# Kernel tuning notes

Hardware: AMD Instinct MI355X
Metric: run time of the kernel (lower is better)

The kernel has to match this reference:

```python
import jax, jax.numpy as jnp
import numpy as np

# Model dims (match init_kwargs / input_specs)
L = 2      # layer_dim
B = 64     # batch
T = 512    # max seq len
D = 256    # input_dim (== hidden_dim, required by stacked wiring)
H = 256    # hidden_dim
O = 2      # output_dim


def setup_inputs() -> dict:
    key = jax.random.key(0)
    ks = jax.random.split(key, 10)
    s = 1.0 / np.sqrt(H)
    f32 = jnp.float32
    return {
        "x_data": jax.random.normal(ks[0], (B, T, D), f32),
        "x_length": jax.random.randint(ks[1], (B,), 1, T + 1),
        "x_label": jax.random.uniform(ks[2], (B,), f32),
        # Per-layer GRU-cell weights, stacked over layers (bias=False).
        "Wz": (jax.random.normal(ks[3], (L, D, H), f32) * s),
        "Uz": (jax.random.normal(ks[4], (L, H, H), f32) * s),
        "Wr": (jax.random.normal(ks[5], (L, D, H), f32) * s),
        "Ur": (jax.random.normal(ks[6], (L, H, H), f32) * s),
        "Wh": (jax.random.normal(ks[7], (L, D, H), f32) * s),
        "Uh": (jax.random.normal(ks[8], (L, H, H), f32) * s),
        # Output projection of the last layer (only last layer's `out` is used).
        "Wo": (jax.random.normal(ks[9], (H, O), f32) * s),
    }


def reference(x_data, x_length, x_label, Wz, Uz, Wr, Ur, Wh, Uh, Wo):
    # Training-mode forward: sum over batch and valid timesteps of
    # (label - sigmoid(out[:, 1]))**2, with per-layer states S1, S2
    # carried across time. Vectorized over batch; lax.scan over time.
    Tn = x_data.shape[1]
    xs = jnp.swapaxes(x_data, 0, 1)  # [T, B, D]
    S1_0 = jnp.zeros((L, B, H), x_data.dtype)
    S2_0 = jnp.zeros((L, B, H), x_data.dtype)

    def step(carry, xt):
        S1, S2 = carry
        inp = xt  # [B, D]
        for l in range(L):  # small fixed layer loop
            z = jax.nn.sigmoid(inp @ Wz[l] + S1[l] @ Uz[l])
            r = jax.nn.sigmoid(inp @ Wr[l] + S1[l] @ Ur[l])
            h = jnp.tanh(inp @ Wh[l] + (r * S1[l]) @ Uh[l])
            hn = (1.0 - z) * S1[l] + z * h          # new hidden (S1)
            S2n = z * S2[l] + (1.0 - z) * h          # secondary memory (S2)
            S1 = S1.at[l].set(hn)
            S2 = S2.at[l].set(S2n)
            inp = hn
        score = jax.nn.sigmoid((inp @ Wo)[:, 1])     # out[:, 1] -> [B]
        return (S1, S2), score

    _, scores = jax.lax.scan(step, (S1_0, S2_0), xs)  # [T, B]
    mask = (jnp.arange(Tn)[:, None] < x_length[None, :]).astype(scores.dtype)
    loss = jnp.sum(mask * (x_label[None, :] - scores) ** 2)
    return loss
```

## Files before the change

kernel.cpp:

```cpp
#include <hip/hip_runtime.h>

#define LAY 2
#define BATCH 64
#define TMAX 512
#define DIM 256
#define AST 264
#define CHUNK 16

typedef float floatx4 __attribute__((ext_vector_type(4)));
typedef __bf16 bf16x8 __attribute__((ext_vector_type(8)));
#define MFMA_FP8  __builtin_amdgcn_mfma_f32_16x16x32_fp8_fp8
#define MFMA_BF16 __builtin_amdgcn_mfma_f32_16x16x32_bf16

#define BAR_LDS() asm volatile("s_waitcnt lgkmcnt(0)\n\ts_barrier" ::: "memory")

#define OFF_WPW 0x60000
#define OFF_FLG 0x150000
#define OFF_XP  0x200000
#define OFF_HP  0x1C00000
#define OFF_HN  0x3600000

__device__ __forceinline__ unsigned short f2bf(float f) {
    unsigned int u = __float_as_uint(f);
    unsigned int r = u + 0x7fffu + ((u >> 16) & 1u);
    return (unsigned short)(r >> 16);
}
__device__ __forceinline__ unsigned int pk2(float a, float b) {
    return (unsigned int)__builtin_amdgcn_cvt_pk_fp8_f32(a, b, 0, false);
}
__device__ __forceinline__ unsigned char f2q(float a) { return (unsigned char)(pk2(a, a) & 0xff); }
__device__ __forceinline__ void unp4(unsigned int u, float* f) {
    auto lo = __builtin_amdgcn_cvt_pk_f32_fp8((int)u, false);
    auto hi = __builtin_amdgcn_cvt_pk_f32_fp8((int)u, true);
    f[0] = lo[0]; f[1] = lo[1]; f[2] = hi[0]; f[3] = hi[1];
}
__device__ __forceinline__ float sigf(float x) {
    return __builtin_amdgcn_rcpf(1.f + __expf(-x));
}
__device__ __forceinline__ float tanhfast2y(float twoy) { return 2.f * sigf(twoy) - 1.f; }

__global__ void prep_weights(const float* __restrict__ Wz, const float* __restrict__ Wr,
                             const float* __restrict__ Wh, const float* __restrict__ Uz,
                             const float* __restrict__ Ur, const float* __restrict__ Uh,
                             unsigned char* __restrict__ ws, float* __restrict__ out) {
    int T = blockIdx.x * 256 + threadIdx.x;
    if (T == 0) out[0] = 0.f;
    if (T < 32) ((int*)(ws + OFF_FLG))[T] = 0;
    if (T < 196608) {
        int e = T & 3, half = (T >> 2) & 1, lane = (T >> 3) & 63;
        int kp = (T >> 9) & 3, nt = (T >> 11) & 15, mu = T >> 15;
        int g = mu % 3, l = mu / 3;
        const float* s = (g == 0 ? Uz : g == 1 ? Ur : Uh) + l * 65536;
        int n  = nt * 16 + (lane & 15);
        int k0 = (2 * kp + half) * 32 + (lane >> 4) * 8 + 2 * e;
        float w0 = s[(k0 << 8) + n] * 8.f;
        float w1 = s[((k0 + 1) << 8) + n] * 8.f;
        int addr = ((mu * 16 + nt) * 4 + kp) * 1024 + lane * 16 + half * 8 + 2 * e;
        *(unsigned short*)(ws + addr) = (unsigned short)(pk2(w0, w1) & 0xffff);
    } else {
        int T2 = T - 196608;
        int e = T2 & 3, lane = (T2 >> 2) & 63;
        int kf = (T2 >> 8) & 7, nt = (T2 >> 11) & 15, mw = T2 >> 15;
        int g = mw % 3, l = mw / 3;
        const float* s = (g == 0 ? Wz : g == 1 ? Wr : Wh) + l * 65536;
        int n  = nt * 16 + (lane & 15);
        int k0 = kf * 32 + (lane >> 4) * 8 + 2 * e;
        unsigned int v = (unsigned int)f2bf(s[(k0 << 8) + n]) |
                         ((unsigned int)f2bf(s[((k0 + 1) << 8) + n]) << 16);
        int addr = ((mw * 16 + nt) * 8 + kf) * 1024 + lane * 16 + 4 * e;
        *(unsigned int*)(ws + OFF_WPW + addr) = v;
    }
}

template <int F32SRC>
__global__ __launch_bounds__(1024) void proj_kernel(const void* __restrict__ src,
                                                    const unsigned char* __restrict__ wpW,
                                                    unsigned int* __restrict__ xpo, int matbase) {
    const int bgt = blockIdx.x;
    const int t = bgt & 511, bg = bgt >> 9;
    const int tid = threadIdx.x, wave = tid >> 6, lane = tid & 63;
    const int l15 = lane & 15, quad = lane >> 4;
    const size_t rowoff = ((size_t)(bg * 16 + l15) * 512 + t) * 256;

    bf16x8 af[8];
    if (F32SRC) {
        const float* s = (const float*)src + rowoff;
#pragma unroll
        for (int kf = 0; kf < 8; ++kf) {
            float4 a = *(const float4*)(s + kf * 32 + quad * 8);
            float4 b = *(const float4*)(s + kf * 32 + quad * 8 + 4);
            union { unsigned short u[8]; bf16x8 v; } cv;
            cv.u[0] = f2bf(a.x); cv.u[1] = f2bf(a.y); cv.u[2] = f2bf(a.z); cv.u[3] = f2bf(a.w);
            cv.u[4] = f2bf(b.x); cv.u[5] = f2bf(b.y); cv.u[6] = f2bf(b.z); cv.u[7] = f2bf(b.w);
            af[kf] = cv.v;
        }
    } else {
        const unsigned short* s = (const unsigned short*)src + rowoff;
#pragma unroll
        for (int kf = 0; kf < 8; ++kf) af[kf] = *(const bf16x8*)(s + kf * 32 + quad * 8);
    }

    floatx4 az = {0.f, 0.f, 0.f, 0.f}, ar = az, ah = az;
    const unsigned char* bz = wpW + (size_t)(((matbase + 0) * 16 + wave) * 8) * 1024 + lane * 16;
    const unsigned char* br = wpW + (size_t)(((matbase + 1) * 16 + wave) * 8) * 1024 + lane * 16;
    const unsigned char* bh = wpW + (size_t)(((matbase + 2) * 16 + wave) * 8) * 1024 + lane * 16;
#pragma unroll
    for (int kf = 0; kf < 8; ++kf) {
        az = MFMA_BF16(af[kf], *(const bf16x8*)(bz + kf * 1024), az, 0, 0, 0);
        ar = MFMA_BF16(af[kf], *(const bf16x8*)(br + kf * 1024), ar, 0, 0, 0);
        ah = MFMA_BF16(af[kf], *(const bf16x8*)(bh + kf * 1024), ah, 0, 0, 0);
    }
    const size_t ob = (size_t)bgt * 3072 + wave * 64 + lane;
    xpo[ob]        = pk2(16.f * az[0], 16.f * az[1]) | (pk2(16.f * az[2], 16.f * az[3]) << 16);
    xpo[ob + 1024] = pk2(16.f * ar[0], 16.f * ar[1]) | (pk2(16.f * ar[2], 16.f * ar[3]) << 16);
    xpo[ob + 2048] = pk2(16.f * ah[0], 16.f * ah[1]) | (pk2(16.f * ah[2], 16.f * ah[3]) << 16);
}

template <int SCORE, int WAIT, int POST>
__device__ __forceinline__ void scan_body(
    const unsigned int* __restrict__ xp, const unsigned char* __restrict__ wpU,
    int lbase, int bg, unsigned short* __restrict__ hnout,
    const int* __restrict__ xlen, const float* __restrict__ xlab,
    const float* __restrict__ Wo, float* __restrict__ out,
    int* wflags, int* pflag,
    unsigned char (*s1q)[AST], unsigned char (*rsq)[AST], float (*s1o)[264],
    float* wo1s, int* s_rdy, int tmax)
{
    const int tid = threadIdx.x, wave = tid >> 6, lane = tid & 63;
    const int l15 = lane & 15, quad = lane >> 4;
    const int b0 = bg * 16;

    for (int i = tid; i < 16 * AST; i += 1024) ((unsigned char*)s1q)[i] = 0;
    if (SCORE && tid < DIM) wo1s[tid] = Wo[2 * tid + 1];
    const int lenr = xlen[b0 + l15];
    const float labr = SCORE ? xlab[b0 + l15] : 0.f;
    (void)lenr; (void)labr;

    const int nt = wave;
    const int colA = nt * 16 + l15, rowb = quad * 4;

    long uz[8], ur[8], uh[8];
    {
        const unsigned char* pz = wpU + (size_t)(((lbase + 0) * 16 + nt) * 4) * 1024 + lane * 16;
        const unsigned char* pr = wpU + (size_t)(((lbase + 1) * 16 + nt) * 4) * 1024 + lane * 16;
        const unsigned char* ph = wpU + (size_t)(((lbase + 2) * 16 + nt) * 4) * 1024 + lane * 16;
#pragma unroll
        for (int kf = 0; kf < 8; ++kf) {
            int o = (kf >> 1) * 1024 + (kf & 1) * 8;
            uz[kf] = *(const long*)(pz + o);
            ur[kf] = *(const long*)(pr + o);
            uh[kf] = *(const long*)(ph + o);
        }
    }
    float s1r[4] = {};
    float accl = 0.f;
    int ready = 0;
    __syncthreads();

    for (int t = 0; t < tmax; ++t) {
        if (WAIT && t >= ready) {
            if (tid == 0) {
                int vv, g = 0;
                for (;;) {
                    int m0 = __hip_atomic_load(wflags + 0, __ATOMIC_RELAXED, __HIP_MEMORY_SCOPE_AGENT);
                    int m1 = __hip_atomic_load(wflags + 1, __ATOMIC_RELAXED, __HIP_MEMORY_SCOPE_AGENT);
                    int m2 = __hip_atomic_load(wflags + 2, __ATOMIC_RELAXED, __HIP_MEMORY_SCOPE_AGENT);
                    int m3 = __hip_atomic_load(wflags + 3, __ATOMIC_RELAXED, __HIP_MEMORY_SCOPE_AGENT);
                    int a = m0 < m1 ? m0 : m1, b = m2 < m3 ? m2 : m3;
                    vv = a < b ? a : b;
                    if (vv > t || ++g > (1 << 19)) break;
                    __builtin_amdgcn_s_sleep(2);
                }
                __threadfence();
                *s_rdy = vv > t ? vv : t + 1;
            }
            __syncthreads();
            ready = *s_rdy;
        }

        const unsigned int* xpt = xp + (size_t)(bg * 512 + t) * 3072 + lane;
        unsigned int xz = xpt[nt * 64];
        unsigned int xr = xpt[1024 + nt * 64];
        unsigned int xh = xpt[2048 + nt * 64];

        long sf[8];
#pragma unroll
        for (int kf = 0; kf < 8; ++kf) sf[kf] = *(const long*)&s1q[l15][kf * 32 + quad * 8];
        floatx4 za = {0.f, 0.f, 0.f, 0.f}, ra = za;
#pragma unroll
        for (int kf = 0; kf < 8; ++kf) {
            ra = MFMA_FP8(sf[kf], ur[kf], ra, 0, 0, 0);
            za = MFMA_FP8(sf[kf], uz[kf], za, 0, 0, 0);
        }
        float xrf[4];
        unp4(xr, xrf);
#pragma unroll
        for (int i = 0; i < 4; ++i) {
            float r = sigf(0.125f * ra[i] + 0.0625f * xrf[i]);
            rsq[rowb + i][colA] = f2q(r * s1r[i]);
        }
        BAR_LDS();

        long rf[8];
#pragma unroll
        for (int kf = 0; kf < 8; ++kf) rf[kf] = *(const long*)&rsq[l15][kf * 32 + quad * 8];
        floatx4 ha = {0.f, 0.f, 0.f, 0.f};
#pragma unroll
        for (int kf = 0; kf < 8; ++kf) ha = MFMA_FP8(rf[kf], uh[kf], ha, 0, 0, 0);
        float xzf[4], xhf[4];
        unp4(xz, xzf); unp4(xh, xhf);
#pragma unroll
        for (int i = 0; i < 4; ++i) {
            float z = sigf(0.125f * za[i] + 0.0625f * xzf[i]);
            float h = tanhfast2y(0.25f * ha[i] + 0.125f * xhf[i]);
            float hn = (1.f - z) * s1r[i] + z * h;
            s1r[i] = hn;
            s1q[rowb + i][colA] = f2q(hn);
            s1o[rowb + i][colA] = hn;
        }
        BAR_LDS();

        if (!SCORE) {
            const int r = tid >> 6, c = (tid & 63) * 4;
            float4 f0 = *(const float4*)&s1o[r][c];
            uint2 o2;
            o2.x = f2bf(f0.x) | ((unsigned)f2bf(f0.y) << 16);
            o2.y = f2bf(f0.z) | ((unsigned)f2bf(f0.w) << 16);
            *(uint2*)(hnout + ((size_t)(b0 + r) * 512 + t) * 256 + c) = o2;
        } else if (wave == 0) {
            const int row = l15, c0 = quad * 64;
            float p = 0.f;
#pragma unroll
            for (int u = 0; u < 64; u += 4) {
                float4 sv = *(const float4*)&s1o[row][c0 + u];
                float4 wv = *(const float4*)&wo1s[c0 + u];
                p = fmaf(sv.x, wv.x, p); p = fmaf(sv.y, wv.y, p);
                p = fmaf(sv.z, wv.z, p); p = fmaf(sv.w, wv.w, p);
            }
            p += __shfl_xor(p, 16);
            p += __shfl_xor(p, 32);
            if (lane < 16 && t < lenr) {
                float sc = sigf(p);
                float d = labr - sc;
                accl = fmaf(d, d, accl);
            }
        }

        if (POST && (((t & (CHUNK - 1)) == (CHUNK - 1)) || t == tmax - 1)) {
            __syncthreads();
            if (tid == 0) {
                __threadfence();
                __hip_atomic_store(pflag, t + 1, __ATOMIC_RELEASE, __HIP_MEMORY_SCOPE_AGENT);
            }
        }
    }

    if (SCORE && wave == 0) {
        accl += __shfl_xor(accl, 1);
        accl += __shfl_xor(accl, 2);
        accl += __shfl_xor(accl, 4);
        accl += __shfl_xor(accl, 8);
        if (lane == 0) atomicAdd(out, accl);
    }
}

__global__ __launch_bounds__(1024, 4) void fused_pipeline(
    const unsigned int* __restrict__ XP, unsigned int* __restrict__ HP,
    const unsigned char* __restrict__ wpU, const unsigned char* __restrict__ wpW,
    unsigned short* __restrict__ HN,
    const int* __restrict__ xlen, const float* __restrict__ xlab,
    const float* __restrict__ Wo, float* __restrict__ out, int* flags)
{
    __shared__ __align__(16) unsigned char s1q[16][AST];
    __shared__ __align__(16) unsigned char rsq[16][AST];
    __shared__ __align__(16) float s1o[16][264];
    __shared__ float wo1s[DIM];
    __shared__ int s_rdy;

    const int bid = blockIdx.x;
    int role, bg, p = 0;
    if (bid < 4)       { role = 0; bg = bid; }
    else if (bid < 20) { role = 1; bg = (bid - 4) >> 2; p = (bid - 4) & 3; }
    else               { role = 2; bg = bid - 20; }

    const int tid = threadIdx.x, wave = tid >> 6, lane = tid & 63;
    const int l15 = lane & 15, quad = lane >> 4;
    const int b0 = bg * 16;

    int v = xlen[b0 + l15];
#pragma unroll
    for (int o = 1; o < 16; o <<= 1) v = max(v, __shfl_xor(v, o));
    const int tmax = __builtin_amdgcn_readfirstlane(v);

    if (role == 0) {
        scan_body<0, 0, 1>(XP, wpU, 0, bg, HN, xlen, xlab, Wo, out,
                           nullptr, flags + bg, s1q, rsq, s1o, wo1s, &s_rdy, tmax);
    } else if (role == 2) {
        scan_body<1, 1, 0>(HP, wpU, 3, bg, nullptr, xlen, xlab, Wo, out,
                           flags + 4 + bg * 4, nullptr, s1q, rsq, s1o, wo1s, &s_rdy, tmax);
    } else {
        int* wf = flags + bg;
        int* pf = flags + 4 + bg * 4 + p;
        const unsigned char* bz = wpW + (size_t)(((3 + 0) * 16 + wave) * 8) * 1024 + lane * 16;
        const unsigned char* br = wpW + (size_t)(((3 + 1) * 16 + wave) * 8) * 1024 + lane * 16;
        const unsigned char* bh = wpW + (size_t)(((3 + 2) * 16 + wave) * 8) * 1024 + lane * 16;
        for (int base = 0; base < tmax; base += CHUNK) {
            const int target = (base + CHUNK < tmax) ? base + CHUNK : tmax;
            if (tid == 0) {
                int vv, g = 0;
                for (;;) {
                    vv = __hip_atomic_load(wf, __ATOMIC_RELAXED, __HIP_MEMORY_SCOPE_AGENT);
                    if (vv >= target || ++g > (1 << 19)) break;
                    __builtin_amdgcn_s_sleep(2);
                }
                __threadfence();
            }
            __syncthreads();

            const int t0 = base + p * 4;
            const int t1 = (t0 + 4 < tmax) ? t0 + 4 : tmax;
            for (int t = t0; t < t1; ++t) {
                const unsigned short* sA = HN + ((size_t)(b0 + l15) * 512 + t) * 256;
                bf16x8 af[8];
#pragma unroll
                for (int kf = 0; kf < 8; ++kf) af[kf] = *(const bf16x8*)(sA + kf * 32 + quad * 8);
                floatx4 az = {0.f, 0.f, 0.f, 0.f}, ar = az, ah = az;
#pragma unroll
                for (int kf = 0; kf < 8; ++kf) {
                    az = MFMA_BF16(af[kf], *(const bf16x8*)(bz + kf * 1024), az, 0, 0, 0);
                    ar = MFMA_BF16(af[kf], *(const bf16x8*)(br + kf * 1024), ar, 0, 0, 0);
                    ah = MFMA_BF16(af[kf], *(const bf16x8*)(bh + kf * 1024), ah, 0, 0, 0);
                }
                const size_t ob = (size_t)(bg * 512 + t) * 3072 + wave * 64 + lane;
                HP[ob]        = pk2(16.f * az[0], 16.f * az[1]) | (pk2(16.f * az[2], 16.f * az[3]) << 16);
                HP[ob + 1024] = pk2(16.f * ar[0], 16.f * ar[1]) | (pk2(16.f * ar[2], 16.f * ar[3]) << 16);
                HP[ob + 2048] = pk2(16.f * ah[0], 16.f * ah[1]) | (pk2(16.f * ah[2], 16.f * ah[3]) << 16);
            }

            __syncthreads();
            if (tid == 0) {
                __threadfence();
                __hip_atomic_store(pf, base + CHUNK, __ATOMIC_RELEASE, __HIP_MEMORY_SCOPE_AGENT);
            }
        }
    }
}

extern "C" void kernel_launch(void* const* d_in, const int* in_sizes, int n_in,
                              void* d_out, int out_size, void* d_ws, size_t ws_size,
                              hipStream_t stream) {
    const float* x    = (const float*)d_in[0];
    const int*   xlen = (const int*)d_in[1];
    const float* xlab = (const float*)d_in[2];
    const float* Wz   = (const float*)d_in[3];
    const float* Uz   = (const float*)d_in[4];
    const float* Wr   = (const float*)d_in[5];
    const float* Ur   = (const float*)d_in[6];
    const float* Wh   = (const float*)d_in[7];
    const float* Uh   = (const float*)d_in[8];
    const float* Wo   = (const float*)d_in[9];
    float* out = (float*)d_out;

    unsigned char* ws  = (unsigned char*)d_ws;
    unsigned char* wpU = ws;
    unsigned char* wpW = ws + OFF_WPW;
    int*           FLG = (int*)(ws + OFF_FLG);
    unsigned int*  XP  = (unsigned int*)(ws + OFF_XP);
    unsigned int*  HP  = (unsigned int*)(ws + OFF_HP);
    unsigned short* HN = (unsigned short*)(ws + OFF_HN);

    prep_weights<<<1536, 256, 0, stream>>>(Wz, Wr, Wh, Uz, Ur, Uh, ws, out);
    proj_kernel<1><<<2048, 1024, 0, stream>>>(x, wpW, XP, 0);
    fused_pipeline<<<24, 1024, 0, stream>>>(XP, HP, wpU, wpW, HN,
                                            xlen, xlab, Wo, out, FLG);
}
```

Before: 1.291 ms.

## Halve scan block to 8 waves with two column tiles each; double projection blocks

The persistent scan blocks drop from 16 waves to 8. Each wave now computes two 16-column tiles of the recurrent GEMMs, and its barriers span half as many waves. The layer-2 input projection blocks per batch group grow from 4 to 8, each handling 2 timesteps per chunk, and the flag layout and wait logic are updated to match. The score reduction is rewritten so every wave handles two batch rows with a full-wave shuffle reduction. The aim is to cut barrier and synchronisation latency on the serial recurrence critical path, at the cost of more registers per wave and less parallelism per step.

```diff
diff --git a/kernel.cpp b/kernel.cpp
--- a/kernel.cpp
+++ b/kernel.cpp
@@ -45,7 +45,7 @@
                              unsigned char* __restrict__ ws, float* __restrict__ out) {
     int T = blockIdx.x * 256 + threadIdx.x;
     if (T == 0) out[0] = 0.f;
-    if (T < 32) ((int*)(ws + OFF_FLG))[T] = 0;
+    if (T < 64) ((int*)(ws + OFF_FLG))[T] = 0;
     if (T < 196608) {
         int e = T & 3, half = (T >> 2) & 1, lane = (T >> 3) & 63;
         int kp = (T >> 9) & 3, nt = (T >> 11) & 15, mu = T >> 15;
@@ -116,7 +116,7 @@
     xpo[ob + 2048] = pk2(16.f * ah[0], 16.f * ah[1]) | (pk2(16.f * ah[2], 16.f * ah[3]) << 16);
 }
 
-template <int SCORE, int WAIT, int POST>
+template <int SCORE, int NWF, int POST>
 __device__ __forceinline__ void scan_body(
     const unsigned int* __restrict__ xp, const unsigned char* __restrict__ wpU,
     int lbase, int bg, unsigned short* __restrict__ hnout,
@@ -130,44 +130,53 @@
     const int l15 = lane & 15, quad = lane >> 4;
     const int b0 = bg * 16;
 
-    for (int i = tid; i < 16 * AST; i += 1024) ((unsigned char*)s1q)[i] = 0;
+    for (int i = tid; i < 16 * AST; i += 512) ((unsigned char*)s1q)[i] = 0;
     if (SCORE && tid < DIM) wo1s[tid] = Wo[2 * tid + 1];
-    const int lenr = xlen[b0 + l15];
-    const float labr = SCORE ? xlab[b0 + l15] : 0.f;
-    (void)lenr; (void)labr;
-
-    const int nt = wave;
-    const int colA = nt * 16 + l15, rowb = quad * 4;
-
-    long uz[8], ur[8], uh[8];
+
+    int len0 = 0, len1 = 0;
+    float lab0 = 0.f, lab1 = 0.f, acc0 = 0.f, acc1 = 0.f;
+    if (SCORE) {
+        len0 = xlen[b0 + wave];     len1 = xlen[b0 + 8 + wave];
+        lab0 = xlab[b0 + wave];     lab1 = xlab[b0 + 8 + wave];
+    }
+
+    const int ntA = wave * 2, ntB = ntA + 1;
+    const int cA = ntA * 16 + l15, cB = cA + 16, rowb = quad * 4;
+
+    long uzA[8], urA[8], uhA[8], uzB[8], urB[8], uhB[8];
     {
-        const unsigned char* pz = wpU + (size_t)(((lbase + 0) * 16 + nt) * 4) * 1024 + lane * 16;
-        const unsigned char* pr = wpU + (size_t)(((lbase + 1) * 16 + nt) * 4) * 1024 + lane * 16;
-        const unsigned char* ph = wpU + (size_t)(((lbase + 2) * 16 + nt) * 4) * 1024 + lane * 16;
+        const unsigned char* pzA = wpU + (size_t)(((lbase + 0) * 16 + ntA) * 4) * 1024 + lane * 16;
+        const unsigned char* prA = wpU + (size_t)(((lbase + 1) * 16 + ntA) * 4) * 1024 + lane * 16;
+        const unsigned char* phA = wpU + (size_t)(((lbase + 2) * 16 + ntA) * 4) * 1024 + lane * 16;
+        const unsigned char* pzB = wpU + (size_t)(((lbase + 0) * 16 + ntB) * 4) * 1024 + lane * 16;
+        const unsigned char* prB = wpU + (size_t)(((lbase + 1) * 16 + ntB) * 4) * 1024 + lane * 16;
+        const unsigned char* phB = wpU + (size_t)(((lbase + 2) * 16 + ntB) * 4) * 1024 + lane * 16;
 #pragma unroll
         for (int kf = 0; kf < 8; ++kf) {
             int o = (kf >> 1) * 1024 + (kf & 1) * 8;
-            uz[kf] = *(const long*)(pz + o);
-            ur[kf] = *(const long*)(pr + o);
-            uh[kf] = *(const long*)(ph + o);
-        }
-    }
-    float s1r[4] = {};
-    float accl = 0.f;
+            uzA[kf] = *(const long*)(pzA + o);
+            urA[kf] = *(const long*)(prA + o);
+            uhA[kf] = *(const long*)(phA + o);
+            uzB[kf] = *(const long*)(pzB + o);
+            urB[kf] = *(const long*)(prB + o);
+            uhB[kf] = *(const long*)(phB + o);
+        }
+    }
+    float s1A[4] = {}, s1B[4] = {};
     int ready = 0;
     __syncthreads();
 
     for (int t = 0; t < tmax; ++t) {
-        if (WAIT && t >= ready) {
+        if (NWF > 0 && t >= ready) {
             if (tid == 0) {
                 int vv, g = 0;
                 for (;;) {
-                    int m0 = __hip_atomic_load(wflags + 0, __ATOMIC_RELAXED, __HIP_MEMORY_SCOPE_AGENT);
-                    int m1 = __hip_atomic_load(wflags + 1, __ATOMIC_RELAXED, __HIP_MEMORY_SCOPE_AGENT);
-                    int m2 = __hip_atomic_load(wflags + 2, __ATOMIC_RELAXED, __HIP_MEMORY_SCOPE_AGENT);
-                    int m3 = __hip_atomic_load(wflags + 3, __ATOMIC_RELAXED, __HIP_MEMORY_SCOPE_AGENT);
-                    int a = m0 < m1 ? m0 : m1, b = m2 < m3 ? m2 : m3;
-                    vv = a < b ? a : b;
+                    vv = 1 << 30;
+#pragma unroll
+                    for (int q = 0; q < (NWF > 0 ? NWF : 1); ++q) {
+                        int m = __hip_atomic_load(wflags + q, __ATOMIC_RELAXED, __HIP_MEMORY_SCOPE_AGENT);
+                        vv = m < vv ? m : vv;
+                    }
                     if (vv > t || ++g > (1 << 19)) break;
                     __builtin_amdgcn_s_sleep(2);
                 }
@@ -179,70 +188,87 @@
         }
 
         const unsigned int* xpt = xp + (size_t)(bg * 512 + t) * 3072 + lane;
-        unsigned int xz = xpt[nt * 64];
-        unsigned int xr = xpt[1024 + nt * 64];
-        unsigned int xh = xpt[2048 + nt * 64];
+        unsigned int xzA = xpt[ntA * 64],        xzB = xpt[ntB * 64];
+        unsigned int xrA = xpt[1024 + ntA * 64], xrB = xpt[1024 + ntB * 64];
+        unsigned int xhA = xpt[2048 + ntA * 64], xhB = xpt[2048 + ntB * 64];
 
         long sf[8];
 #pragma unroll
         for (int kf = 0; kf < 8; ++kf) sf[kf] = *(const long*)&s1q[l15][kf * 32 + quad * 8];
-        floatx4 za = {0.f, 0.f, 0.f, 0.f}, ra = za;
+        floatx4 zer = {0.f, 0.f, 0.f, 0.f};
+        floatx4 raA = zer, raB = zer, zaA = zer, zaB = zer;
 #pragma unroll
         for (int kf = 0; kf < 8; ++kf) {
-            ra = MFMA_FP8(sf[kf], ur[kf], ra, 0, 0, 0);
-            za = MFMA_FP8(sf[kf], uz[kf], za, 0, 0, 0);
-        }
-        float xrf[4];
-        unp4(xr, xrf);
+            raA = MFMA_FP8(sf[kf], urA[kf], raA, 0, 0, 0);
+            raB = MFMA_FP8(sf[kf], urB[kf], raB, 0, 0, 0);
+            zaA = MFMA_FP8(sf[kf], uzA[kf], zaA, 0, 0, 0);
+            zaB = MFMA_FP8(sf[kf], uzB[kf], zaB, 0, 0, 0);
+        }
+        float xrfA[4], xrfB[4];
+        unp4(xrA, xrfA); unp4(xrB, xrfB);
 #pragma unroll
         for (int i = 0; i < 4; ++i) {
-            float r = sigf(0.125f * ra[i] + 0.0625f * xrf[i]);
-            rsq[rowb + i][colA] = f2q(r * s1r[i]);
+            float rA_ = sigf(0.125f * raA[i] + 0.0625f * xrfA[i]);
+            float rB_ = sigf(0.125f * raB[i] + 0.0625f * xrfB[i]);
+            rsq[rowb + i][cA] = f2q(rA_ * s1A[i]);
+            rsq[rowb + i][cB] = f2q(rB_ * s1B[i]);
         }
         BAR_LDS();
 
         long rf[8];
 #pragma unroll
         for (int kf = 0; kf < 8; ++kf) rf[kf] = *(const long*)&rsq[l15][kf * 32 + quad * 8];
-        floatx4 ha = {0.f, 0.f, 0.f, 0.f};
-#pragma unroll
-        for (int kf = 0; kf < 8; ++kf) ha = MFMA_FP8(rf[kf], uh[kf], ha, 0, 0, 0);
-        float xzf[4], xhf[4];
-        unp4(xz, xzf); unp4(xh, xhf);
+        floatx4 haA = zer, haB = zer;
+#pragma unroll
+        for (int kf = 0; kf < 8; ++kf) {
+            haA = MFMA_FP8(rf[kf], uhA[kf], haA, 0, 0, 0);
+            haB = MFMA_FP8(rf[kf], uhB[kf], haB, 0, 0, 0);
+        }
+        float xzfA[4], xzfB[4], xhfA[4], xhfB[4];
+        unp4(xzA, xzfA); unp4(xzB, xzfB); unp4(xhA, xhfA); unp4(xhB, xhfB);
 #pragma unroll
         for (int i = 0; i < 4; ++i) {
-            float z = sigf(0.125f * za[i] + 0.0625f * xzf[i]);
-            float h = tanhfast2y(0.25f * ha[i] + 0.125f * xhf[i]);
-            float hn = (1.f - z) * s1r[i] + z * h;
-            s1r[i] = hn;
-            s1q[rowb + i][colA] = f2q(hn);
-            s1o[rowb + i][colA] = hn;
+            float zA_ = sigf(0.125f * zaA[i] + 0.0625f * xzfA[i]);
+            float hA_ = tanhfast2y(0.25f * haA[i] + 0.125f * xhfA[i]);
+            float hnA = (1.f - zA_) * s1A[i] + zA_ * hA_;
+            s1A[i] = hnA;
+            s1q[rowb + i][cA] = f2q(hnA);
+            s1o[rowb + i][cA] = hnA;
+            float zB_ = sigf(0.125f * zaB[i] + 0.0625f * xzfB[i]);
+            float hB_ = tanhfast2y(0.25f * haB[i] + 0.125f * xhfB[i]);
+            float hnB = (1.f - zB_) * s1B[i] + zB_ * hB_;
+            s1B[i] = hnB;
+            s1q[rowb + i][cB] = f2q(hnB);
+            s1o[rowb + i][cB] = hnB;
         }
         BAR_LDS();
 
         if (!SCORE) {
-            const int r = tid >> 6, c = (tid & 63) * 4;
+            const int r = tid >> 5, c = (tid & 31) * 8;
             float4 f0 = *(const float4*)&s1o[r][c];
-            uint2 o2;
-            o2.x = f2bf(f0.x) | ((unsigned)f2bf(f0.y) << 16);
-            o2.y = f2bf(f0.z) | ((unsigned)f2bf(f0.w) << 16);
-            *(uint2*)(hnout + ((size_t)(b0 + r) * 512 + t) * 256 + c) = o2;
-        } else if (wave == 0) {
-            const int row = l15, c0 = quad * 64;
-            float p = 0.f;
-#pragma unroll
-            for (int u = 0; u < 64; u += 4) {
-                float4 sv = *(const float4*)&s1o[row][c0 + u];
-                float4 wv = *(const float4*)&wo1s[c0 + u];
-                p = fmaf(sv.x, wv.x, p); p = fmaf(sv.y, wv.y, p);
-                p = fmaf(sv.z, wv.z, p); p = fmaf(sv.w, wv.w, p);
-            }
-            p += __shfl_xor(p, 16);
-            p += __shfl_xor(p, 32);
-            if (lane < 16 && t < lenr) {
-                float sc = sigf(p);
-                float d = labr - sc;
-                accl = fmaf(d, d, accl);
+            float4 f1 = *(const float4*)&s1o[r][c + 4];
+            uint4 o4;
+            o4.x = f2bf(f0.x) | ((unsigned)f2bf(f0.y) << 16);
+            o4.y = f2bf(f0.z) | ((unsigned)f2bf(f0.w) << 16);
+            o4.z = f2bf(f1.x) | ((unsigned)f2bf(f1.y) << 16);
+            o4.w = f2bf(f1.z) | ((unsigned)f2bf(f1.w) << 16);
+            *(uint4*)(hnout + ((size_t)(b0 + r) * 512 + t) * 256 + c) = o4;
+        } else {
+            const float4 wv = *(const float4*)&wo1s[lane * 4];
+            const float4 s0 = *(const float4*)&s1o[wave][lane * 4];
+            const float4 s1v = *(const float4*)&s1o[8 + wave][lane * 4];
+            float p0 = s0.x * wv.x;  p0 = fmaf(s0.y, wv.y, p0);
+            p0 = fmaf(s0.z, wv.z, p0); p0 = fmaf(s0.w, wv.w, p0);
+            float p1 = s1v.x * wv.x; p1 = fmaf(s1v.y, wv.y, p1);
+            p1 = fmaf(s1v.z, wv.z, p1); p1 = fmaf(s1v.w, wv.w, p1);
+#pragma unroll
+            for (int o = 1; o < 64; o <<= 1) {
+                p0 += __shfl_xor(p0, o);
+                p1 += __shfl_xor(p1, o);
+            }
+            if (lane == 0) {
+                if (t < len0) { float sc = sigf(p0); float d = lab0 - sc; acc0 = fmaf(d, d, acc0); }
+                if (t < len1) { float sc = sigf(p1); float d = lab1 - sc; acc1 = fmaf(d, d, acc1); }
             }
         }
 
@@ -255,16 +281,10 @@
         }
     }
 
-    if (SCORE && wave == 0) {
-        accl += __shfl_xor(accl, 1);
-        accl += __shfl_xor(accl, 2);
-        accl += __shfl_xor(accl, 4);
-        accl += __shfl_xor(accl, 8);
-        if (lane == 0) atomicAdd(out, accl);
-    }
-}
-
-__global__ __launch_bounds__(1024, 4) void fused_pipeline(
+    if (SCORE && lane == 0) atomicAdd(out, acc0 + acc1);
+}
+
+__global__ __launch_bounds__(512, 2) void fused_pipeline(
     const unsigned int* __restrict__ XP, unsigned int* __restrict__ HP,
     const unsigned char* __restrict__ wpU, const unsigned char* __restrict__ wpW,
     unsigned short* __restrict__ HN,
@@ -280,8 +300,8 @@
     const int bid = blockIdx.x;
     int role, bg, p = 0;
     if (bid < 4)       { role = 0; bg = bid; }
-    else if (bid < 20) { role = 1; bg = (bid - 4) >> 2; p = (bid - 4) & 3; }
-    else               { role = 2; bg = bid - 20; }
+    else if (bid < 36) { role = 1; bg = (bid - 4) >> 3; p = (bid - 4) & 7; }
+    else               { role = 2; bg = bid - 36; }
 
     const int tid = threadIdx.x, wave = tid >> 6, lane = tid & 63;
     const int l15 = lane & 15, quad = lane >> 4;
@@ -296,14 +316,18 @@
         scan_body<0, 0, 1>(XP, wpU, 0, bg, HN, xlen, xlab, Wo, out,
                            nullptr, flags + bg, s1q, rsq, s1o, wo1s, &s_rdy, tmax);
     } else if (role == 2) {
-        scan_body<1, 1, 0>(HP, wpU, 3, bg, nullptr, xlen, xlab, Wo, out,
-                           flags + 4 + bg * 4, nullptr, s1q, rsq, s1o, wo1s, &s_rdy, tmax);
+        scan_body<1, 8, 0>(HP, wpU, 3, bg, nullptr, xlen, xlab, Wo, out,
+                           flags + 4 + bg * 8, nullptr, s1q, rsq, s1o, wo1s, &s_rdy, tmax);
     } else {
         int* wf = flags + bg;
-        int* pf = flags + 4 + bg * 4 + p;
-        const unsigned char* bz = wpW + (size_t)(((3 + 0) * 16 + wave) * 8) * 1024 + lane * 16;
-        const unsigned char* br = wpW + (size_t)(((3 + 1) * 16 + wave) * 8) * 1024 + lane * 16;
-        const unsigned char* bh = wpW + (size_t)(((3 + 2) * 16 + wave) * 8) * 1024 + lane * 16;
+        int* pf = flags + 4 + bg * 8 + p;
+        const int ntA = wave * 2, ntB = ntA + 1;
+        const unsigned char* bzA = wpW + (size_t)(((3 + 0) * 16 + ntA) * 8) * 1024 + lane * 16;
+        const unsigned char* brA = wpW + (size_t)(((3 + 1) * 16 + ntA) * 8) * 1024 + lane * 16;
+        const unsigned char* bhA = wpW + (size_t)(((3 + 2) * 16 + ntA) * 8) * 1024 + lane * 16;
+        const unsigned char* bzB = wpW + (size_t)(((3 + 0) * 16 + ntB) * 8) * 1024 + lane * 16;
+        const unsigned char* brB = wpW + (size_t)(((3 + 1) * 16 + ntB) * 8) * 1024 + lane * 16;
+        const unsigned char* bhB = wpW + (size_t)(((3 + 2) * 16 + ntB) * 8) * 1024 + lane * 16;
         for (int base = 0; base < tmax; base += CHUNK) {
             const int target = (base + CHUNK < tmax) ? base + CHUNK : tmax;
             if (tid == 0) {
@@ -317,24 +341,32 @@
             }
             __syncthreads();
 
-            const int t0 = base + p * 4;
-            const int t1 = (t0 + 4 < tmax) ? t0 + 4 : tmax;
+            const int t0 = base + p * 2;
+            const int t1 = (t0 + 2 < tmax) ? t0 + 2 : tmax;
             for (int t = t0; t < t1; ++t) {
                 const unsigned short* sA = HN + ((size_t)(b0 + l15) * 512 + t) * 256;
                 bf16x8 af[8];
 #pragma unroll
                 for (int kf = 0; kf < 8; ++kf) af[kf] = *(const bf16x8*)(sA + kf * 32 + quad * 8);
-                floatx4 az = {0.f, 0.f, 0.f, 0.f}, ar = az, ah = az;
+                floatx4 zer = {0.f, 0.f, 0.f, 0.f};
+                floatx4 azA = zer, arA = zer, ahA = zer, azB = zer, arB = zer, ahB = zer;
 #pragma unroll
                 for (int kf = 0; kf < 8; ++kf) {
-                    az = MFMA_BF16(af[kf], *(const bf16x8*)(bz + kf * 1024), az, 0, 0, 0);
-                    ar = MFMA_BF16(af[kf], *(const bf16x8*)(br + kf * 1024), ar, 0, 0, 0);
-                    ah = MFMA_BF16(af[kf], *(const bf16x8*)(bh + kf * 1024), ah, 0, 0, 0);
+                    azA = MFMA_BF16(af[kf], *(const bf16x8*)(bzA + kf * 1024), azA, 0, 0, 0);
+                    arA = MFMA_BF16(af[kf], *(const bf16x8*)(brA + kf * 1024), arA, 0, 0, 0);
+                    ahA = MFMA_BF16(af[kf], *(const bf16x8*)(bhA + kf * 1024), ahA, 0, 0, 0);
+                    azB = MFMA_BF16(af[kf], *(const bf16x8*)(bzB + kf * 1024), azB, 0, 0, 0);
+                    arB = MFMA_BF16(af[kf], *(const bf16x8*)(brB + kf * 1024), arB, 0, 0, 0);
+                    ahB = MFMA_BF16(af[kf], *(const bf16x8*)(bhB + kf * 1024), ahB, 0, 0, 0);
                 }
-                const size_t ob = (size_t)(bg * 512 + t) * 3072 + wave * 64 + lane;
-                HP[ob]        = pk2(16.f * az[0], 16.f * az[1]) | (pk2(16.f * az[2], 16.f * az[3]) << 16);
-                HP[ob + 1024] = pk2(16.f * ar[0], 16.f * ar[1]) | (pk2(16.f * ar[2], 16.f * ar[3]) << 16);
-                HP[ob + 2048] = pk2(16.f * ah[0], 16.f * ah[1]) | (pk2(16.f * ah[2], 16.f * ah[3]) << 16);
+                const size_t obA = (size_t)(bg * 512 + t) * 3072 + ntA * 64 + lane;
+                const size_t obB = obA + 64;
+                HP[obA]        = pk2(16.f * azA[0], 16.f * azA[1]) | (pk2(16.f * azA[2], 16.f * azA[3]) << 16);
+                HP[obA + 1024] = pk2(16.f * arA[0], 16.f * arA[1]) | (pk2(16.f * arA[2], 16.f * arA[3]) << 16);
+                HP[obA + 2048] = pk2(16.f * ahA[0], 16.f * ahA[1]) | (pk2(16.f * ahA[2], 16.f * ahA[3]) << 16);
+                HP[obB]        = pk2(16.f * azB[0], 16.f * azB[1]) | (pk2(16.f * azB[2], 16.f * azB[3]) << 16);
+                HP[obB + 1024] = pk2(16.f * arB[0], 16.f * arB[1]) | (pk2(16.f * arB[2], 16.f * arB[3]) << 16);
+                HP[obB + 2048] = pk2(16.f * ahB[0], 16.f * ahB[1]) | (pk2(16.f * ahB[2], 16.f * ahB[3]) << 16);
             }
 
             __syncthreads();
@@ -371,6 +403,6 @@
 
     prep_weights<<<1536, 256, 0, stream>>>(Wz, Wr, Wh, Uz, Ur, Uh, ws, out);
     proj_kernel<1><<<2048, 1024, 0, stream>>>(x, wpW, XP, 0);
-    fused_pipeline<<<24, 1024, 0, stream>>>(XP, HP, wpU, wpW, HN,
-                                            xlen, xlab, Wo, out, FLG);
-}
+    fused_pipeline<<<40, 512, 0, stream>>>(XP, HP, wpU, wpW, HN,
+                                           xlen, xlab, Wo, out, FLG);
+}
```

Result: slower. 1.511 ms (+17.0%).

## Fold layer-0 input projection into persistent pipeline as flag-signaled producer blocks

Applied to the files above, without the earlier changes.

Removes the separate proj_kernel launch and adds four producer blocks inside fused_pipeline that compute the layer-0 input projection in chunks and publish progress through flags. The layer-0 scan blocks now wait on those flags, so the projection overlaps the recurrence instead of running as a whole-device pass before it. The trade-off is that only four blocks now do the projection work that the 2048-block launch used to do. If the producers fall behind the serial scan, they become a new bottleneck.

```diff
diff --git a/kernel.cpp b/kernel.cpp
--- a/kernel.cpp
+++ b/kernel.cpp
@@ -72,51 +72,7 @@
     }
 }
 
-template <int F32SRC>
-__global__ __launch_bounds__(1024) void proj_kernel(const void* __restrict__ src,
-                                                    const unsigned char* __restrict__ wpW,
-                                                    unsigned int* __restrict__ xpo, int matbase) {
-    const int bgt = blockIdx.x;
-    const int t = bgt & 511, bg = bgt >> 9;
-    const int tid = threadIdx.x, wave = tid >> 6, lane = tid & 63;
-    const int l15 = lane & 15, quad = lane >> 4;
-    const size_t rowoff = ((size_t)(bg * 16 + l15) * 512 + t) * 256;
-
-    bf16x8 af[8];
-    if (F32SRC) {
-        const float* s = (const float*)src + rowoff;
-#pragma unroll
-        for (int kf = 0; kf < 8; ++kf) {
-            float4 a = *(const float4*)(s + kf * 32 + quad * 8);
-            float4 b = *(const float4*)(s + kf * 32 + quad * 8 + 4);
-            union { unsigned short u[8]; bf16x8 v; } cv;
-            cv.u[0] = f2bf(a.x); cv.u[1] = f2bf(a.y); cv.u[2] = f2bf(a.z); cv.u[3] = f2bf(a.w);
-            cv.u[4] = f2bf(b.x); cv.u[5] = f2bf(b.y); cv.u[6] = f2bf(b.z); cv.u[7] = f2bf(b.w);
-            af[kf] = cv.v;
-        }
-    } else {
-        const unsigned short* s = (const unsigned short*)src + rowoff;
-#pragma unroll
-        for (int kf = 0; kf < 8; ++kf) af[kf] = *(const bf16x8*)(s + kf * 32 + quad * 8);
-    }
-
-    floatx4 az = {0.f, 0.f, 0.f, 0.f}, ar = az, ah = az;
-    const unsigned char* bz = wpW + (size_t)(((matbase + 0) * 16 + wave) * 8) * 1024 + lane * 16;
-    const unsigned char* br = wpW + (size_t)(((matbase + 1) * 16 + wave) * 8) * 1024 + lane * 16;
-    const unsigned char* bh = wpW + (size_t)(((matbase + 2) * 16 + wave) * 8) * 1024 + lane * 16;
-#pragma unroll
-    for (int kf = 0; kf < 8; ++kf) {
-        az = MFMA_BF16(af[kf], *(const bf16x8*)(bz + kf * 1024), az, 0, 0, 0);
-        ar = MFMA_BF16(af[kf], *(const bf16x8*)(br + kf * 1024), ar, 0, 0, 0);
-        ah = MFMA_BF16(af[kf], *(const bf16x8*)(bh + kf * 1024), ah, 0, 0, 0);
-    }
-    const size_t ob = (size_t)bgt * 3072 + wave * 64 + lane;
-    xpo[ob]        = pk2(16.f * az[0], 16.f * az[1]) | (pk2(16.f * az[2], 16.f * az[3]) << 16);
-    xpo[ob + 1024] = pk2(16.f * ar[0], 16.f * ar[1]) | (pk2(16.f * ar[2], 16.f * ar[3]) << 16);
-    xpo[ob + 2048] = pk2(16.f * ah[0], 16.f * ah[1]) | (pk2(16.f * ah[2], 16.f * ah[3]) << 16);
-}
-
-template <int SCORE, int WAIT, int POST>
+template <int SCORE, int NWF, int POST>
 __device__ __forceinline__ void scan_body(
     const unsigned int* __restrict__ xp, const unsigned char* __restrict__ wpU,
     int lbase, int bg, unsigned short* __restrict__ hnout,
@@ -158,24 +114,26 @@
     __syncthreads();
 
     for (int t = 0; t < tmax; ++t) {
-        if (WAIT && t >= ready) {
-            if (tid == 0) {
-                int vv, g = 0;
-                for (;;) {
-                    int m0 = __hip_atomic_load(wflags + 0, __ATOMIC_RELAXED, __HIP_MEMORY_SCOPE_AGENT);
-                    int m1 = __hip_atomic_load(wflags + 1, __ATOMIC_RELAXED, __HIP_MEMORY_SCOPE_AGENT);
-                    int m2 = __hip_atomic_load(wflags + 2, __ATOMIC_RELAXED, __HIP_MEMORY_SCOPE_AGENT);
-                    int m3 = __hip_atomic_load(wflags + 3, __ATOMIC_RELAXED, __HIP_MEMORY_SCOPE_AGENT);
-                    int a = m0 < m1 ? m0 : m1, b = m2 < m3 ? m2 : m3;
-                    vv = a < b ? a : b;
-                    if (vv > t || ++g > (1 << 19)) break;
-                    __builtin_amdgcn_s_sleep(2);
-                }
-                __threadfence();
-                *s_rdy = vv > t ? vv : t + 1;
-            }
-            __syncthreads();
-            ready = *s_rdy;
+        if constexpr (NWF > 0) {
+            if (t >= ready) {
+                if (tid == 0) {
+                    int vv, g = 0;
+                    for (;;) {
+                        vv = 1 << 30;
+#pragma unroll
+                        for (int q = 0; q < NWF; ++q) {
+                            int m = __hip_atomic_load(wflags + q, __ATOMIC_RELAXED, __HIP_MEMORY_SCOPE_AGENT);
+                            vv = m < vv ? m : vv;
+                        }
+                        if (vv > t || ++g > (1 << 19)) break;
+                        __builtin_amdgcn_s_sleep(2);
+                    }
+                    __threadfence();
+                    *s_rdy = vv > t ? vv : t + 1;
+                }
+                __syncthreads();
+                ready = *s_rdy;
+            }
         }
 
         const unsigned int* xpt = xp + (size_t)(bg * 512 + t) * 3072 + lane;
@@ -265,7 +223,8 @@
 }
 
 __global__ __launch_bounds__(1024, 4) void fused_pipeline(
-    const unsigned int* __restrict__ XP, unsigned int* __restrict__ HP,
+    const float* __restrict__ x,
+    unsigned int* __restrict__ XP, unsigned int* __restrict__ HP,
     const unsigned char* __restrict__ wpU, const unsigned char* __restrict__ wpW,
     unsigned short* __restrict__ HN,
     const int* __restrict__ xlen, const float* __restrict__ xlab,
@@ -280,8 +239,9 @@
     const int bid = blockIdx.x;
     int role, bg, p = 0;
     if (bid < 4)       { role = 0; bg = bid; }
-    else if (bid < 20) { role = 1; bg = (bid - 4) >> 2; p = (bid - 4) & 3; }
-    else               { role = 2; bg = bid - 20; }
+    else if (bid < 8)  { role = 1; bg = bid - 4; }
+    else if (bid < 24) { role = 2; bg = (bid - 8) >> 2; p = (bid - 8) & 3; }
+    else               { role = 3; bg = bid - 24; }
 
     const int tid = threadIdx.x, wave = tid >> 6, lane = tid & 63;
     const int l15 = lane & 15, quad = lane >> 4;
@@ -293,14 +253,51 @@
     const int tmax = __builtin_amdgcn_readfirstlane(v);
 
     if (role == 0) {
-        scan_body<0, 0, 1>(XP, wpU, 0, bg, HN, xlen, xlab, Wo, out,
-                           nullptr, flags + bg, s1q, rsq, s1o, wo1s, &s_rdy, tmax);
-    } else if (role == 2) {
-        scan_body<1, 1, 0>(HP, wpU, 3, bg, nullptr, xlen, xlab, Wo, out,
-                           flags + 4 + bg * 4, nullptr, s1q, rsq, s1o, wo1s, &s_rdy, tmax);
+        int* pf = flags + bg;
+        const unsigned char* bz = wpW + (size_t)((0 * 16 + wave) * 8) * 1024 + lane * 16;
+        const unsigned char* br = wpW + (size_t)((1 * 16 + wave) * 8) * 1024 + lane * 16;
+        const unsigned char* bh = wpW + (size_t)((2 * 16 + wave) * 8) * 1024 + lane * 16;
+        for (int base = 0; base < tmax; base += CHUNK) {
+            const int t1 = (base + CHUNK < tmax) ? base + CHUNK : tmax;
+            for (int t = base; t < t1; ++t) {
+                const float* s = x + ((size_t)(b0 + l15) * 512 + t) * 256;
+                bf16x8 af[8];
+#pragma unroll
+                for (int kf = 0; kf < 8; ++kf) {
+                    float4 a = *(const float4*)(s + kf * 32 + quad * 8);
+                    float4 b = *(const float4*)(s + kf * 32 + quad * 8 + 4);
+                    union { unsigned short u[8]; bf16x8 v; } cv;
+                    cv.u[0] = f2bf(a.x); cv.u[1] = f2bf(a.y); cv.u[2] = f2bf(a.z); cv.u[3] = f2bf(a.w);
+                    cv.u[4] = f2bf(b.x); cv.u[5] = f2bf(b.y); cv.u[6] = f2bf(b.z); cv.u[7] = f2bf(b.w);
+                    af[kf] = cv.v;
+                }
+                floatx4 az = {0.f, 0.f, 0.f, 0.f}, ar = az, ah = az;
+#pragma unroll
+                for (int kf = 0; kf < 8; ++kf) {
+                    az = MFMA_BF16(af[kf], *(const bf16x8*)(bz + kf * 1024), az, 0, 0, 0);
+                    ar = MFMA_BF16(af[kf], *(const bf16x8*)(br + kf * 1024), ar, 0, 0, 0);
+                    ah = MFMA_BF16(af[kf], *(const bf16x8*)(bh + kf * 1024), ah, 0, 0, 0);
+                }
+                const size_t ob = (size_t)(bg * 512 + t) * 3072 + wave * 64 + lane;
+                XP[ob]        = pk2(16.f * az[0], 16.f * az[1]) | (pk2(16.f * az[2], 16.f * az[3]) << 16);
+                XP[ob + 1024] = pk2(16.f * ar[0], 16.f * ar[1]) | (pk2(16.f * ar[2], 16.f * ar[3]) << 16);
+                XP[ob + 2048] = pk2(16.f * ah[0], 16.f * ah[1]) | (pk2(16.f * ah[2], 16.f * ah[3]) << 16);
+            }
+            __syncthreads();
+            if (tid == 0) {
+                __threadfence();
+                __hip_atomic_store(pf, base + CHUNK, __ATOMIC_RELEASE, __HIP_MEMORY_SCOPE_AGENT);
+            }
+        }
+    } else if (role == 1) {
+        scan_body<0, 1, 1>(XP, wpU, 0, bg, HN, xlen, xlab, Wo, out,
+                           flags + bg, flags + 4 + bg, s1q, rsq, s1o, wo1s, &s_rdy, tmax);
+    } else if (role == 3) {
+        scan_body<1, 4, 0>(HP, wpU, 3, bg, nullptr, xlen, xlab, Wo, out,
+                           flags + 8 + bg * 4, nullptr, s1q, rsq, s1o, wo1s, &s_rdy, tmax);
     } else {
-        int* wf = flags + bg;
-        int* pf = flags + 4 + bg * 4 + p;
+        int* wf = flags + 4 + bg;
+        int* pf = flags + 8 + bg * 4 + p;
         const unsigned char* bz = wpW + (size_t)(((3 + 0) * 16 + wave) * 8) * 1024 + lane * 16;
         const unsigned char* br = wpW + (size_t)(((3 + 1) * 16 + wave) * 8) * 1024 + lane * 16;
         const unsigned char* bh = wpW + (size_t)(((3 + 2) * 16 + wave) * 8) * 1024 + lane * 16;
@@ -370,7 +367,6 @@
     unsigned short* HN = (unsigned short*)(ws + OFF_HN);
 
     prep_weights<<<1536, 256, 0, stream>>>(Wz, Wr, Wh, Uz, Ur, Uh, ws, out);
-    proj_kernel<1><<<2048, 1024, 0, stream>>>(x, wpW, XP, 0);
-    fused_pipeline<<<24, 1024, 0, stream>>>(XP, HP, wpU, wpW, HN,
+    fused_pipeline<<<28, 1024, 0, stream>>>(x, XP, HP, wpU, wpW, HN,
                                             xlen, xlab, Wo, out, FLG);
 }
```

Result: slower. 5.130 ms (+297.4%).
